# Performance work log

Hardware: AMD Instinct MI355X
Metric: run time of the kernel (lower is better)

## Reference

```python
import jax, jax.numpy as jnp
import numpy as np

DIM = 128; DSTATE = 64; DHEAD = 64; EXPAND = 2
DINNER = EXPAND * DIM; NH = DINNER // DHEAD
CONVK = 4; CHUNK = 128
BATCH = 1; DD = 32; HH = 32; WW = 32
CONVCH = DINNER + 2 * DSTATE
DPROJ = 2 * DINNER + 2 * DSTATE + NH


def rmsnorm(v, w, eps=1e-6):
    return v * jax.lax.rsqrt(jnp.mean(v * v, axis=-1, keepdims=True) + eps) * w


def ssd(xh, dt, A, Bm, Cm):
    # chunked SSD selective scan. xh [b,l,h,p], dt [b,l,h], A [h], Bm/Cm [b,l,n]
    b, l, h, p = xh.shape
    n = Bm.shape[-1]
    c, k = l // CHUNK, CHUNK
    dA = (dt * A).reshape(b, c, k, h)
    xdt = (xh * dt[..., None]).reshape(b, c, k, h, p)
    Bm = Bm.reshape(b, c, k, n)
    Cm = Cm.reshape(b, c, k, n)
    cum = jnp.cumsum(dA, axis=2)                  # [b,c,k,h] inclusive
    cum_h = cum.transpose(0, 1, 3, 2)             # [b,c,h,k]
    tri = jnp.tril(jnp.ones((k, k), bool))
    Lmat = jnp.exp(jnp.where(tri, cum_h[..., :, None] - cum_h[..., None, :], -jnp.inf))
    CB = jnp.einsum('bctn,bcsn->bcts', Cm, Bm)
    Y_intra = jnp.einsum('bcts,bchts,bcshp->bcthp', CB, Lmat, xdt)
    decay_end = jnp.exp(cum[:, :, -1:, :] - cum)  # [b,c,k,h]
    S = jnp.einsum('bcsn,bcsh,bcshp->bchpn', Bm, decay_end, xdt)
    cdec = jnp.exp(cum[:, :, -1])                 # [b,c,h]

    def step(hprev, inp):
        s_c, dec = inp
        return dec[:, :, None, None] * hprev + s_c, hprev

    init = jnp.zeros((b, h, p, n), xh.dtype)
    _, hprevs = jax.lax.scan(step, init, (S.transpose(1, 0, 2, 3, 4), cdec.transpose(1, 0, 2)))
    hprevs = hprevs.transpose(1, 0, 2, 3, 4)      # [b,c,h,p,n] state at each chunk start
    Y_inter = jnp.einsum('bctn,bcth,bchpn->bcthp', Cm, jnp.exp(cum), hprevs)
    return (Y_intra + Y_inter).reshape(b, l, h, p)


def mamba2(x, Win, convw, convb, dtb, Alog, Dp, normw, Wout):
    b, l, _ = x.shape
    zxbcdt = x @ Win
    z = zxbcdt[..., :DINNER]
    xBC = zxbcdt[..., DINNER:DINNER + CONVCH]
    dt = zxbcdt[..., DINNER + CONVCH:]
    xc = xBC.transpose(0, 2, 1)
    xc = jax.lax.conv_general_dilated(xc, convw, (1,), [(CONVK - 1, 0)],
                                      dimension_numbers=('NCH', 'OIH', 'NCH'),
                                      feature_group_count=CONVCH)
    xBC = jax.nn.silu(xc + convb[None, :, None]).transpose(0, 2, 1)
    xh = xBC[..., :DINNER].reshape(b, l, NH, DHEAD)
    Bm = xBC[..., DINNER:DINNER + DSTATE]
    Cm = xBC[..., DINNER + DSTATE:]
    dt = jax.nn.softplus(dt + dtb)
    A = -jnp.exp(Alog)
    y = ssd(xh, dt, A, Bm, Cm) + Dp[None, None, :, None] * xh
    y = y.reshape(b, l, DINNER)
    y = rmsnorm(y * jax.nn.silu(z), normw)
    return y @ Wout


def ss3d(xn, gate_w, gate_b, ps, pn, pz):
    B, D, H, W, C = xn.shape
    x_s = xn.reshape(B, -1, C)
    x_n = jnp.transpose(xn, (0, 2, 1, 3, 4)).reshape(B, -1, C)
    x_z = jnp.transpose(xn, (0, 3, 1, 2, 4)).reshape(B, -1, C)
    o_sf = mamba2(x_s, *ps).reshape(B, D, H, W, C)
    o_sb = jnp.flip(mamba2(jnp.flip(x_s, 1), *ps), 1).reshape(B, D, H, W, C)
    o_nf = mamba2(x_n, *pn).reshape(B, H, D, W, C).transpose(0, 2, 1, 3, 4)
    o_nb = jnp.flip(mamba2(jnp.flip(x_n, 1), *pn), 1).reshape(B, H, D, W, C).transpose(0, 2, 1, 3, 4)
    o_zf = mamba2(x_z, *pz).reshape(B, W, D, H, C).transpose(0, 2, 3, 1, 4)
    o_zb = jnp.flip(mamba2(jnp.flip(x_z, 1), *pz), 1).reshape(B, W, D, H, C).transpose(0, 2, 3, 1, 4)
    stack = jnp.stack([o_sf, o_sb, o_nf, o_nb, o_zf, o_zb], axis=1)  # [B,6,D,H,W,C]
    gates = jax.nn.softmax(xn @ gate_w + gate_b, axis=-1)            # [B,D,H,W,6]
    gates = jnp.transpose(gates[..., None], (0, 4, 1, 2, 3, 5))      # [B,6,D,H,W,1]
    return (stack * gates).sum(axis=1)


def block(x, norm_w, gate_w, gate_b, ps, pn, pz, loc_dw_w, loc_dw_b, loc_pw_w, loc_pw_b,
          ca_w1, ca_b1, ca_w2, ca_b2, alpha):
    xp = jnp.transpose(x, (0, 2, 3, 4, 1))
    xn = rmsnorm(xp, norm_w)
    g = jnp.transpose(ss3d(xn, gate_w, gate_b, ps, pn, pz), (0, 4, 1, 2, 3))
    xcf = jnp.transpose(xn, (0, 4, 1, 2, 3))
    lc = jax.lax.conv_general_dilated(xcf, loc_dw_w, (1, 1, 1), [(1, 1)] * 3,
                                      dimension_numbers=('NCDHW', 'OIDHW', 'NCDHW'),
                                      feature_group_count=DIM) + loc_dw_b[None, :, None, None, None]
    lc = jax.nn.silu(jnp.einsum('bcdhw,oc->bodhw', lc, loc_pw_w) + loc_pw_b[None, :, None, None, None])
    fused = alpha * g + (1.0 - alpha) * lc
    yc = jnp.mean(fused, axis=(2, 3, 4), keepdims=True)
    yc = jnp.einsum('bcdhw,oc->bodhw', yc, ca_w1) + ca_b1[None, :, None, None, None]
    yc = jnp.where(yc >= 0, yc, 0.1 * yc)  # LeakyReLU(0.1)
    yc = jnp.einsum('bcdhw,oc->bodhw', yc, ca_w2) + ca_b2[None, :, None, None, None]
    return x + fused * jax.nn.sigmoid(yc)


def setup_inputs() -> dict:
    keys = iter(jax.random.split(jax.random.key(0), 64))

    def rn(shape, s=1.0):
        return jax.random.normal(next(keys), shape, jnp.float32) * s

    inp = {"x": rn((BATCH, DIM, DD, HH, WW))}
    inp["norm_w"] = jnp.ones((DIM,)) + rn((DIM,), 0.02)
    inp["gate_w"] = rn((DIM, 6), 0.02)
    inp["gate_b"] = jnp.zeros((6,))
    for m in ("s", "n", "zm"):
        inp[m + "_Win"] = rn((DIM, DPROJ), 0.02)
        inp[m + "_convw"] = rn((CONVCH, 1, CONVK), 0.2)
        inp[m + "_convb"] = jnp.zeros((CONVCH,))
        inp[m + "_dtb"] = rn((NH,), 0.3)
        inp[m + "_Alog"] = jnp.log(jnp.arange(1, NH + 1, dtype=jnp.float32))
        inp[m + "_D"] = jnp.ones((NH,))
        inp[m + "_normw"] = jnp.ones((DINNER,))
        inp[m + "_Wout"] = rn((DINNER, DIM), 0.02)
    inp["loc_dw_w"] = rn((DIM, 1, 3, 3, 3), 0.1)
    inp["loc_dw_b"] = jnp.zeros((DIM,))
    inp["loc_pw_w"] = rn((DIM, DIM), 0.05)
    inp["loc_pw_b"] = jnp.zeros((DIM,))
    inp["ca_w1"] = rn((DIM // 16, DIM), 0.05)
    inp["ca_b1"] = jnp.zeros((DIM // 16,))
    inp["ca_w2"] = rn((DIM, DIM // 16), 0.05)
    inp["ca_b2"] = jnp.zeros((DIM,))
    inp["alpha"] = jnp.array(0.5, jnp.float32)
    return inp


def reference(x, norm_w, gate_w, gate_b,
              s_Win, s_convw, s_convb, s_dtb, s_Alog, s_D, s_normw, s_Wout,
              n_Win, n_convw, n_convb, n_dtb, n_Alog, n_D, n_normw, n_Wout,
              zm_Win, zm_convw, zm_convb, zm_dtb, zm_Alog, zm_D, zm_normw, zm_Wout,
              loc_dw_w, loc_dw_b, loc_pw_w, loc_pw_b, ca_w1, ca_b1, ca_w2, ca_b2, alpha):
    ps = (s_Win, s_convw, s_convb, s_dtb, s_Alog, s_D, s_normw, s_Wout)
    pn = (n_Win, n_convw, n_convb, n_dtb, n_Alog, n_D, n_normw, n_Wout)
    pz = (zm_Win, zm_convw, zm_convb, zm_dtb, zm_Alog, zm_D, zm_normw, zm_Wout)
    return block(x, norm_w, gate_w, gate_b, ps, pn, pz,
                 loc_dw_w, loc_dw_b, loc_pw_w, loc_pw_b, ca_w1, ca_b1, ca_w2, ca_b2, alpha)
```

## Files before the change

### kernel.cpp

```cpp
#include <hip/hip_runtime.h>


typedef unsigned short u16;
typedef unsigned int   u32;
typedef __attribute__((ext_vector_type(8))) short short8;
typedef __attribute__((ext_vector_type(8))) _Float16 half8;
typedef __attribute__((ext_vector_type(4))) float f32x4;

#define LSEQ 32768
#define CDIM 128
#define NPROJ 644
#define CCH 384
#define DIN 256
#define NHD 4
#define CKL 128
#define NCHK 256

__device__ __forceinline__ float b2f(u16 u){ u32 x=((u32)u)<<16; float f; __builtin_memcpy(&f,&x,4); return f; }
__device__ __forceinline__ u16 f2b(float f){ u32 x; __builtin_memcpy(&x,&f,4); x += 0x7fffu + ((x>>16)&1u); return (u16)(x>>16); }
__device__ __forceinline__ u16 f2h(float v){ _Float16 h=(_Float16)v; u16 b; __builtin_memcpy(&b,&h,2); return b; }
__device__ __forceinline__ float h2f(u16 b){ _Float16 h; __builtin_memcpy(&h,&b,2); return (float)h; }
__device__ __forceinline__ void up4(uint2 v, float* o){
  union { uint2 u; _Float16 h[4]; } c; c.u = v;
  o[0]=(float)c.h[0]; o[1]=(float)c.h[1]; o[2]=(float)c.h[2]; o[3]=(float)c.h[3];
}
__device__ __forceinline__ uint2 pk4(const float* o){
  union { uint2 u; _Float16 h[4]; } c;
  c.h[0]=(_Float16)o[0]; c.h[1]=(_Float16)o[1]; c.h[2]=(_Float16)o[2]; c.h[3]=(_Float16)o[3];
  return c.u;
}
__device__ __forceinline__ float sigmoidf_(float v){ return 1.f/(1.f+__expf(-v)); }
__device__ __forceinline__ float siluf_(float v){ return v*sigmoidf_(v); }
__device__ __forceinline__ float softplusf_(float v){ return (v>20.f)? v : log1pf(__expf(v)); }

__device__ __forceinline__ int seq2sp(int t, int run){
  int te = (run&1) ? (LSEQ-1-t) : t;
  int a = te>>10, b=(te>>5)&31, c=te&31;
  int d,h,w;
  switch(run>>1){
    case 0: d=a; h=b; w=c; break;
    case 1: h=a; d=b; w=c; break;
    default: w=a; d=b; h=c; break;
  }
  return (d<<10)|(h<<5)|w;
}

__global__ void k_xn(const float* __restrict__ x, const float* __restrict__ nw, float* __restrict__ XN){
  int s = blockIdx.x*256 + threadIdx.x;
  float ss = 0.f;
  #pragma unroll 8
  for (int c=0;c<CDIM;c++){ float v=x[c*LSEQ+s]; ss += v*v; }
  float sc = rsqrtf(ss*(1.f/CDIM)+1e-6f);
  #pragma unroll 8
  for (int c=0;c<CDIM;c++){ XN[c*LSEQ+s] = x[c*LSEQ+s]*sc*nw[c]; }
}

__global__ void k_gates(const float* __restrict__ XN, const float* __restrict__ gw, const float* __restrict__ gb, float* __restrict__ G){
  int s = blockIdx.x*256 + threadIdx.x;
  float a[6];
  #pragma unroll
  for (int j=0;j<6;j++) a[j]=gb[j];
  for (int c=0;c<CDIM;c++){
    float v = XN[c*LSEQ+s];
    #pragma unroll
    for (int j=0;j<6;j++) a[j] += v*gw[c*6+j];
  }
  float m=a[0];
  #pragma unroll
  for (int j=1;j<6;j++) m = fmaxf(m,a[j]);
  float e[6], ssum=0.f;
  #pragma unroll
  for (int j=0;j<6;j++){ e[j]=__expf(a[j]-m); ssum+=e[j]; }
  float inv = 1.f/ssum;
  #pragma unroll
  for (int j=0;j<6;j++) G[j*LSEQ+s] = e[j]*inv;
}

__global__ __launch_bounds__(256) void k_permute(const float* __restrict__ XN, u16* __restrict__ XNT, int dir){
  __shared__ u16 TS[128*34];
  int a = blockIdx.x>>5, b = blockIdx.x&31;
  int tid = threadIdx.x;
  int spa = (dir==1)? b : a;
  int spb = (dir==1)? a : b;
  int spbase = spa*1024 + spb*32;
  for (int idx=tid; idx<4096; idx+=256){
    int c = idx>>5, i = idx&31;
    TS[c*34+i] = f2b(XN[c*LSEQ + spbase + i]);
  }
  __syncthreads();
  for (int idx=tid; idx<4096; idx+=256){
    int i = idx>>7, c = idx&127;
    int t = (dir==2) ? (i*1024 + a*32 + b) : (a*1024 + b*32 + i);
    XNT[t*128 + c] = TS[c*34+i];
  }
}

__global__ void k_prepw(const float* __restrict__ Win, u16* __restrict__ WinT){
  int idx = blockIdx.x*256 + threadIdx.x;
  int j = idx>>7, k = idx&127;
  float v = (j<NPROJ)? Win[k*NPROJ + j] : 0.f;
  WinT[idx] = f2b(v);
}

__global__ void k_prewo(const float* __restrict__ Wout, u16* __restrict__ WoT){
  int idx = blockIdx.x*256 + threadIdx.x;
  int c = idx>>8, k = idx&255;
  WoT[idx] = f2h(Wout[k*CDIM + c]);
}

__global__ __launch_bounds__(256) void k_gin_mfma(const u16* __restrict__ XNT, const u16* __restrict__ WinT,
                                                  u16* __restrict__ ZX, int flip){
  __shared__ u16 Asb[128*136];
  __shared__ u16 Bsb[128*136];
  int j0 = blockIdx.x*128, t0 = blockIdx.y*128;
  int tid = threadIdx.x;
  for (int ch = tid; ch < 2048; ch += 256){
    int row = ch>>4, c8 = ch&15;
    int tg = flip ? (LSEQ-1-(t0+row)) : (t0+row);
    uint4 av = *(const uint4*)(XNT + tg*128 + c8*8);
    *(uint4*)(&Asb[row*136 + c8*8]) = av;
    uint4 bv = *(const uint4*)(WinT + (j0+row)*128 + c8*8);
    *(uint4*)(&Bsb[row*136 + c8*8]) = bv;
  }
  __syncthreads();
  int lane = tid&63, wid = tid>>6;
  int wm = (wid>>1)*64, wn = (wid&1)*64;
  int lm = lane&15, lq = lane>>4;
  f32x4 acc[4][4] = {};
  for (int kt=0; kt<4; kt++){
    short8 af[4], bf[4];
    #pragma unroll
    for (int mt=0;mt<4;mt++) af[mt] = *(const short8*)(&Asb[(wm+mt*16+lm)*136 + kt*32 + lq*8]);
    #pragma unroll
    for (int nt=0;nt<4;nt++) bf[nt] = *(const short8*)(&Bsb[(wn+nt*16+lm)*136 + kt*32 + lq*8]);
    #pragma unroll
    for (int mt=0;mt<4;mt++)
      #pragma unroll
      for (int nt=0;nt<4;nt++)
        acc[mt][nt] = __builtin_amdgcn_mfma_f32_16x16x32_bf16(af[mt], bf[nt], acc[mt][nt], 0,0,0);
  }
  #pragma unroll
  for (int mt=0;mt<4;mt++){
    #pragma unroll
    for (int nt=0;nt<4;nt++){
      int j = j0 + wn + nt*16 + lm;
      if (j < NPROJ){
        #pragma unroll
        for (int r=0;r<4;r++){
          int t = t0 + wm + mt*16 + lq*4 + r;
          ZX[t*NPROJ + j] = f2h(acc[mt][nt][r]);
        }
      }
    }
  }
}

__global__ __launch_bounds__(384) void k_conv(const u16* __restrict__ ZX, const float* __restrict__ cw,
                                              const float* __restrict__ cb, u16* __restrict__ XB){
  __shared__ u16 smc[35*384];
  int t0 = blockIdx.x*32;
  int tid = threadIdx.x;
  for (int idx=tid; idx<13440; idx+=384){
    int j = idx/384, chh = idx - j*384;
    int t = t0-3+j;
    smc[idx] = (t>=0)? ZX[t*NPROJ + 256 + chh] : (u16)0;
  }
  __syncthreads();
  int ch = tid;
  float w0=cw[ch*4], w1=cw[ch*4+1], w2=cw[ch*4+2], w3=cw[ch*4+3], bb=cb[ch];
  for (int i=0;i<32;i++){
    float acc = w0*h2f(smc[i*384+ch]) + w1*h2f(smc[(i+1)*384+ch])
              + w2*h2f(smc[(i+2)*384+ch]) + w3*h2f(smc[(i+3)*384+ch]) + bb;
    XB[(t0+i)*CCH + ch] = f2h(siluf_(acc));
  }
}

__global__ __launch_bounds__(256) void k_dtcum(const u16* __restrict__ ZX, const float* __restrict__ dtb,
                                               const float* __restrict__ Alog, float* __restrict__ DT,
                                               float* __restrict__ CUM, float* __restrict__ CDEC,
                                               float* __restrict__ DE){
  int g = blockIdx.x*4 + (threadIdx.x>>6);
  int lane = threadIdx.x&63;
  int c = g>>2, h = g&3;
  float A = -__expf(Alog[h]);
  float bias = dtb[h];
  int t0 = c*CKL + lane*2;
  float x0 = h2f(ZX[t0*NPROJ + 640 + h]);
  float x1 = h2f(ZX[(t0+1)*NPROJ + 640 + h]);
  float d0 = softplusf_(x0+bias), d1 = softplusf_(x1+bias);
  DT[t0*4+h] = d0; DT[(t0+1)*4+h] = d1;
  float e0 = d0*A, e1 = d1*A;
  float s = e0+e1;
  #pragma unroll
  for (int off=1; off<64; off<<=1){
    float v = __shfl_up(s, off, 64);
    if (lane>=off) s += v;
  }
  float c0 = s - e1, c1 = s;
  CUM[t0*4+h] = c0;
  CUM[(t0+1)*4+h] = c1;
  float tot = __shfl(s, 63, 64);
  DE[t0*4+h]     = __expf(tot - c0);
  DE[(t0+1)*4+h] = __expf(tot - c1);
  if (lane==0) CDEC[c*4+h] = __expf(tot);
}

__global__ __launch_bounds__(256,4) void k_chunk(const u16* __restrict__ XB, const float* __restrict__ DT,
                                                 const float* __restrict__ CUM, const float* __restrict__ DE,
                                                 const float* __restrict__ Dp,
                                                 u16* __restrict__ YA, u16* __restrict__ ST){
  __shared__ u16 sh[19968];
  u16* R0   = sh;
  u16* Cs   = sh;
  u16* Bs   = sh + 5120;
  u16* Mtri = sh;
  u16* Xsh  = sh + 11264;

  int bid = blockIdx.x; int c = bid&255, h = bid>>8;
  int tid = threadIdx.x, lane = tid&63, wid = tid>>6;
  int lm = lane&15, lq = lane>>4;
  const u16* XBc = XB + c*CKL*CCH;
  const float* DTc = DT + c*CKL*4 + h;
  const float* DEc = DE + c*CKL*4 + h;

  for (int idx=tid; idx<4096; idx+=256){
    int t2 = idx>>6, n = idx&63, t = t2*2;
    const u16* r0 = XBc + t*CCH;
    float dt0 = DTc[t*4], dt1 = DTc[(t+1)*4];
    u32 xp = (u32)f2h(h2f(r0[(h<<6)+n])*dt0) | ((u32)f2h(h2f(r0[CCH+(h<<6)+n])*dt1)<<16);
    *(u32*)&Xsh[n*136 + t] = xp;
    float de0 = DEc[t*4], de1 = DEc[(t+1)*4];
    u32 bp = (u32)f2h(h2f(r0[256+n])*de0) | ((u32)f2h(h2f(r0[CCH+256+n])*de1)<<16);
    *(u32*)&R0[n*136 + t] = bp;
  }
  if (tid<128) ((float*)(Xsh + (tid>>1)*136 + 128))[tid&1] = CUM[(c*CKL+tid)*4 + h];
  __syncthreads();
  #define CUMS(t) (((const float*)(Xsh + ((t)>>1)*136 + 128))[(t)&1])

  uint4 stg[4];
  #pragma unroll
  for (int q=0;q<4;q++){
    int idx = tid + q*256;
    int mat = idx>>9, r = (idx>>2)&127, qq = idx&3;
    stg[q] = *(const uint4*)(XBc + r*CCH + (mat? 256:320) + qq*8);
  }
  f32x4 sa[4] = {};
  #pragma unroll
  for (int kt=0; kt<4; kt++){
    half8 aa = *(const half8*)&Xsh[(wid*16+lm)*136 + kt*32 + lq*8];
    #pragma unroll
    for (int nt=0;nt<4;nt++){
      half8 bq = *(const half8*)&R0[(nt*16+lm)*136 + kt*32 + lq*8];
      sa[nt] = __builtin_amdgcn_mfma_f32_16x16x32_f16(aa, bq, sa[nt], 0,0,0);
    }
  }
  #pragma unroll
  for (int nt=0;nt<4;nt++){
    int n = nt*16 + lm;
    #pragma unroll
    for (int r=0;r<4;r++){
      int p = wid*16 + lq*4 + r;
      ST[((c*4+h)*64 + p)*64 + n] = f2h(sa[nt][r]);
    }
  }
  __syncthreads();

  #pragma unroll
  for (int q=0;q<4;q++){
    int idx = tid + q*256;
    int mat = idx>>9, r = (idx>>2)&127, qq = idx&3;
    *(uint4*)&R0[(mat?5120:0) + r*40 + qq*8] = stg[q];
  }
  __syncthreads();

  int sp0 = wid, sp1 = 7 - wid;
  #pragma unroll
  for (int q=0;q<4;q++){
    int idx = tid + q*256;
    int mat = idx>>9, r = (idx>>2)&127, qq = idx&3;
    stg[q] = *(const uint4*)(XBc + r*CCH + (mat? 256:320) + 32 + qq*8);
  }
  f32x4 cbA[4] = {};
  f32x4 cbB[8] = {};
  {
    half8 afA = *(const half8*)&Cs[(sp0*16+lm)*40 + lq*8];
    half8 afB = *(const half8*)&Cs[(sp1*16+lm)*40 + lq*8];
    #pragma unroll
    for (int st=0; st<8; st++){
      if (st <= sp1){
        half8 bq = *(const half8*)&Bs[(st*16+lm)*40 + lq*8];
        if (st <= sp0)
          cbA[st&3] = __builtin_amdgcn_mfma_f32_16x16x32_f16(afA, bq, cbA[st&3], 0,0,0);
        cbB[st] = __builtin_amdgcn_mfma_f32_16x16x32_f16(afB, bq, cbB[st], 0,0,0);
      }
    }
  }
  __syncthreads();

  #pragma unroll
  for (int q=0;q<4;q++){
    int idx = tid + q*256;
    int mat = idx>>9, r = (idx>>2)&127, qq = idx&3;
    *(uint4*)&R0[(mat?5120:0) + r*40 + qq*8] = stg[q];
  }
  __syncthreads();

  {
    half8 afA = *(const half8*)&Cs[(sp0*16+lm)*40 + lq*8];
    half8 afB = *(const half8*)&Cs[(sp1*16+lm)*40 + lq*8];
    #pragma unroll
    for (int st=0; st<8; st++){
      if (st <= sp1){
        half8 bq = *(const half8*)&Bs[(st*16+lm)*40 + lq*8];
        if (st <= sp0)
          cbA[st&3] = __builtin_amdgcn_mfma_f32_16x16x32_f16(afA, bq, cbA[st&3], 0,0,0);
        cbB[st] = __builtin_amdgcn_mfma_f32_16x16x32_f16(afB, bq, cbB[st], 0,0,0);
      }
    }
  }
  __syncthreads();

  float dval = Dp[h];
  #pragma unroll
  for (int i=0;i<2;i++){
    int sp_ = i ? sp1 : sp0;
    int q = sp_ >> 1;
    int Wst = 32*q + 40;
    int mb  = 16*(32*q*q + 48*q + (sp_&1)*(32*q+40));
    u16* Mrow = Mtri + mb;
    float ct[4];
    #pragma unroll
    for (int r=0;r<4;r++) ct[r] = CUMS(sp_*16 + lq*4 + r);

    #pragma unroll
    for (int st=0; st<8; st++){
      if (st <= sp_){
        int s = st*16 + lm;
        float cs = CUMS(s);
        f32x4 cb;
        if (i==0) cb = cbA[st&3]; else cb = cbB[st];
        if (st == sp_){
          #pragma unroll
          for (int r=0;r<4;r++){
            int t = sp_*16 + lq*4 + r;
            float m = (s <= t) ? cb[r]*__expf(ct[r]-cs) : 0.f;
            Mrow[(lq*4+r)*Wst + s] = f2h(m);
          }
          if (!(sp_&1)){
            #pragma unroll
            for (int r=0;r<4;r++) Mrow[(lq*4+r)*Wst + s + 16] = 0;
          }
        } else {
          #pragma unroll
          for (int r=0;r<4;r++)
            Mrow[(lq*4+r)*Wst + s] = f2h(cb[r]*__expf(ct[r]-cs));
        }
      }
    }

    f32x4 ya[4] = {};
    int nkt = q + 1;
    #pragma unroll
    for (int kt=0; kt<4; kt++){
      if (kt < nkt){
        half8 af = *(const half8*)&Mrow[lm*Wst + kt*32 + lq*8];
        #pragma unroll
        for (int nt=0;nt<4;nt++){
          half8 bq = *(const half8*)&Xsh[(nt*16+lm)*136 + kt*32 + lq*8];
          ya[nt] = __builtin_amdgcn_mfma_f32_16x16x32_f16(af, bq, ya[nt], 0,0,0);
        }
      }
    }

    #pragma unroll
    for (int nt=0;nt<4;nt++){
      int p = nt*16 + lm;
      #pragma unroll
      for (int r=0;r<4;r++){
        int t = sp_*16 + lq*4 + r;
        float xhv = h2f(XBc[t*CCH + (h<<6) + p]);
        YA[((c*CKL+t)<<8) + (h<<6) + p] = f2h(ya[nt][r] + dval*xhv);
      }
    }
  }
  #undef CUMS
}

__global__ void k_scan(const u16* __restrict__ ST, u16* __restrict__ HP, const float* __restrict__ CDEC){
  int g = blockIdx.x*256 + threadIdx.x;
  int h = g>>12;
  float hp = 0.f;
  #pragma unroll 8
  for (int c=0;c<NCHK;c++){
    float dec = CDEC[(c<<2)+h];
    float sv = h2f(ST[g + (c<<14)]);
    HP[g + (c<<14)] = f2h(hp);
    hp = dec*hp + sv;
  }
}

__global__ __launch_bounds__(256) void k_inter(const u16* __restrict__ XB, const float* __restrict__ CUM,
                                               const u16* __restrict__ HP, u16* __restrict__ YB){
  __shared__ u16 Cs[128*72];
  __shared__ u16 Hs[4*64*72];
  __shared__ float ex_s[4*128];
  int c = blockIdx.x;
  int tid = threadIdx.x, lane = tid&63, wid = tid>>6;
  int lm = lane&15, lq = lane>>4;
  for (int idx=tid; idx<1024; idx+=256){
    int t = idx>>3, b8 = idx&7;
    *(uint4*)&Cs[t*72 + b8*8] = *(const uint4*)(XB + (c*CKL+t)*CCH + 320 + b8*8);
  }
  for (int idx=tid; idx<2048; idx+=256){
    int h = idx>>9, p = (idx>>3)&63, b8 = idx&7;
    *(uint4*)&Hs[(h*64+p)*72 + b8*8] = *(const uint4*)(HP + ((c*4+h)*64+p)*64 + b8*8);
  }
  for (int idx=tid; idx<512; idx+=256){
    int h = idx>>7, t = idx&127;
    ex_s[h*128+t] = __expf(CUM[(c*CKL+t)*4+h]);
  }
  __syncthreads();
  int h = wid;
  const u16* Hh = &Hs[h*64*72];
  f32x4 acc[8][4] = {};
  for (int kt=0; kt<2; kt++){
    half8 af[8], bfv[4];
    #pragma unroll
    for (int mt=0;mt<8;mt++) af[mt] = *(const half8*)&Cs[(mt*16+lm)*72 + kt*32 + lq*8];
    #pragma unroll
    for (int nt=0;nt<4;nt++) bfv[nt] = *(const half8*)&Hh[(nt*16+lm)*72 + kt*32 + lq*8];
    #pragma unroll
    for (int mt=0;mt<8;mt++)
      #pragma unroll
      for (int nt=0;nt<4;nt++)
        acc[mt][nt] = __builtin_amdgcn_mfma_f32_16x16x32_f16(af[mt], bfv[nt], acc[mt][nt], 0,0,0);
  }
  #pragma unroll
  for (int mt=0;mt<8;mt++){
    #pragma unroll
    for (int r=0;r<4;r++){
      int t = mt*16 + lq*4 + r;
      float e = ex_s[h*128+t];
      u16* dst = &YB[((c*CKL+t)<<8) + (h<<6)];
      #pragma unroll
      for (int nt=0;nt<4;nt++){
        int p = nt*16 + lm;
        dst[p] = f2h(e*acc[mt][nt][r]);
      }
    }
  }
}

__global__ __launch_bounds__(256) void k_ynorm(const u16* __restrict__ YA, const u16* __restrict__ YB,
                                               const u16* __restrict__ ZX, const float* __restrict__ nw,
                                               u16* __restrict__ YH){
  int t = blockIdx.x*4 + (threadIdx.x>>6);
  int lane = threadIdx.x&63;
  float a[4], b[4], z[4], u[4];
  up4(*(const uint2*)(YA + t*DIN + lane*4), a);
  up4(*(const uint2*)(YB + t*DIN + lane*4), b);
  up4(*(const uint2*)(ZX + t*NPROJ + lane*4), z);
  float4 w = *(const float4*)(nw + lane*4);
  float ss = 0.f;
  #pragma unroll
  for (int j=0;j<4;j++){ u[j] = (a[j]+b[j])*siluf_(z[j]); ss += u[j]*u[j]; }
  #pragma unroll
  for (int off=32; off; off>>=1) ss += __shfl_xor(ss, off, 64);
  float sc = rsqrtf(ss*(1.f/DIN)+1e-6f);
  float o[4] = { u[0]*sc*w.x, u[1]*sc*w.y, u[2]*sc*w.z, u[3]*sc*w.w };
  *(uint2*)(YH + t*DIN + lane*4) = pk4(o);
}

__global__ __launch_bounds__(256) void k_gout_mfma(const u16* __restrict__ YH, const u16* __restrict__ WoT,
                                                   const float* __restrict__ G, float* __restrict__ GACC, int run){
  __shared__ u16 Ys[128*136];
  __shared__ u16 Ws[128*136];
  int t0 = blockIdx.x*128;
  int tid = threadIdx.x, lane = tid&63, wid = tid>>6;
  int lm = lane&15, lq = lane>>4;
  f32x4 acc[2][8] = {};
  for (int kb=0; kb<2; kb++){
    __syncthreads();
    for (int ch=tid; ch<2048; ch+=256){
      int row = ch>>4, c8 = ch&15;
      *(uint4*)&Ys[row*136 + c8*8] = *(const uint4*)(YH + (t0+row)*DIN + kb*128 + c8*8);
      *(uint4*)&Ws[row*136 + c8*8] = *(const uint4*)(WoT + row*DIN + kb*128 + c8*8);
    }
    __syncthreads();
    for (int kt=0; kt<4; kt++){
      half8 af[2], bfv[8];
      #pragma unroll
      for (int mt=0;mt<2;mt++) af[mt] = *(const half8*)&Ys[(wid*32+mt*16+lm)*136 + kt*32 + lq*8];
      #pragma unroll
      for (int nt=0;nt<8;nt++) bfv[nt] = *(const half8*)&Ws[(nt*16+lm)*136 + kt*32 + lq*8];
      #pragma unroll
      for (int mt=0;mt<2;mt++)
        #pragma unroll
        for (int nt=0;nt<8;nt++)
          acc[mt][nt] = __builtin_amdgcn_mfma_f32_16x16x32_f16(af[mt], bfv[nt], acc[mt][nt], 0,0,0);
    }
  }
  #pragma unroll
  for (int mt=0;mt<2;mt++){
    #pragma unroll
    for (int r=0;r<4;r++){
      int t = t0 + wid*32 + mt*16 + lq*4 + r;
      int sp = seq2sp(t, run);
      float g = G[run*LSEQ + sp];
      float* dst = &GACC[sp*CDIM];
      if (run==0){
        #pragma unroll
        for (int nt=0;nt<8;nt++) dst[nt*16+lm] = g*acc[mt][nt][r];
      } else {
        #pragma unroll
        for (int nt=0;nt<8;nt++) dst[nt*16+lm] += g*acc[mt][nt][r];
      }
    }
  }
}

__global__ __launch_bounds__(256) void k_dwconv(const float* __restrict__ XN, const float* __restrict__ w,
                                                const float* __restrict__ b, float* __restrict__ LC1){
  __shared__ float sm[3*34*40];
  int cc = blockIdx.x>>5, d = blockIdx.x&31;
  int tid = threadIdx.x;
  for (int i=tid; i<4080; i+=256) sm[i] = 0.f;
  __syncthreads();
  #pragma unroll
  for (int p=0;p<3;p++){
    int dz = d-1+p;
    if ((unsigned)dz<=31u){
      for (int idx=tid; idx<1024; idx+=256){
        int hh = idx>>5, ww = idx&31;
        sm[p*1360 + (hh+1)*40 + (ww+4)] = XN[cc*LSEQ + (dz<<10) + idx];
      }
    }
  }
  __syncthreads();
  float wreg[27];
  #pragma unroll
  for (int i=0;i<27;i++) wreg[i] = w[cc*27+i];
  float bias = b[cc];
  int h = tid>>3, w0 = (tid&7)*4;
  float4 acc = {bias,bias,bias,bias};
  #pragma unroll
  for (int p=0;p<3;p++){
    #pragma unroll
    for (int dy=0;dy<3;dy++){
      const float* row = &sm[p*1360 + (h+dy)*40 + 4];
      float left  = row[w0-1];
      float4 mid  = *(const float4*)&row[w0];
      float right = row[w0+4];
      float wa=wreg[p*9+dy*3+0], wb=wreg[p*9+dy*3+1], wc=wreg[p*9+dy*3+2];
      acc.x += wa*left  + wb*mid.x + wc*mid.y;
      acc.y += wa*mid.x + wb*mid.y + wc*mid.z;
      acc.z += wa*mid.y + wb*mid.z + wc*mid.w;
      acc.w += wa*mid.z + wb*mid.w + wc*right;
    }
  }
  *(float4*)&LC1[cc*LSEQ + (d<<10) + h*32 + w0] = acc;
}

__global__ __launch_bounds__(256) void k_pw(const float* __restrict__ LC1, const float* __restrict__ pw,
                                            const float* __restrict__ pwb, float* __restrict__ LC2){
  __shared__ u16 Ws[128*136];
  __shared__ u16 Bs[128*136];
  int s0 = blockIdx.x*128;
  int tid = threadIdx.x, lane = tid&63, wid = tid>>6;
  int lm = lane&15, lq = lane>>4;
  for (int idx=tid; idx<16384; idx+=256){
    int o = idx>>7, cc = idx&127;
    Ws[o*136+cc] = f2h(pw[idx]);
  }
  for (int idx=tid; idx<16384; idx+=256){
    int cc = idx>>7, n = idx&127;
    Bs[n*136+cc] = f2h(LC1[cc*LSEQ + s0 + n]);
  }
  __syncthreads();
  f32x4 acc[2][8] = {};
  for (int kt=0; kt<4; kt++){
    half8 af[2], bfv[8];
    #pragma unroll
    for (int mt=0;mt<2;mt++) af[mt] = *(const half8*)&Ws[(wid*32+mt*16+lm)*136 + kt*32 + lq*8];
    #pragma unroll
    for (int nt=0;nt<8;nt++) bfv[nt] = *(const half8*)&Bs[(nt*16+lm)*136 + kt*32 + lq*8];
    #pragma unroll
    for (int mt=0;mt<2;mt++)
      #pragma unroll
      for (int nt=0;nt<8;nt++)
        acc[mt][nt] = __builtin_amdgcn_mfma_f32_16x16x32_f16(af[mt], bfv[nt], acc[mt][nt], 0,0,0);
  }
  #pragma unroll
  for (int mt=0;mt<2;mt++){
    #pragma unroll
    for (int r=0;r<4;r++){
      int o = wid*32 + mt*16 + lq*4 + r;
      float bb = pwb[o];
      float* dst = &LC2[o*LSEQ + s0];
      #pragma unroll
      for (int nt=0;nt<8;nt++){
        int n = nt*16 + lm;
        dst[n] = siluf_(acc[mt][nt][r] + bb);
      }
    }
  }
}

__global__ void k_fuse(const float* __restrict__ GACC, const float* __restrict__ LC2,
                       const float* __restrict__ alpha, float* __restrict__ FUSED){
  __shared__ float tile[64*65];
  int bs = blockIdx.x>>1, bc = blockIdx.x&1;
  int s0 = bs*64, c0 = bc*64;
  int tid = threadIdx.x;
  float a = alpha[0];
  for (int idx=tid; idx<4096; idx+=256){
    int i = idx>>6, j = idx&63;
    tile[i*65+j] = GACC[(s0+i)*CDIM + c0+j];
  }
  __syncthreads();
  for (int idx=tid; idx<4096; idx+=256){
    int j = idx>>6, i = idx&63;
    float g = tile[i*65+j];
    float l = LC2[(c0+j)*LSEQ + s0+i];
    FUSED[(c0+j)*LSEQ + s0+i] = a*g + (1.f-a)*l;
  }
}

__global__ void k_mean(const float* __restrict__ F, float* __restrict__ MEAN){
  __shared__ float red[4];
  int cc = blockIdx.x, tid = threadIdx.x;
  float acc = 0.f;
  for (int s=tid; s<LSEQ; s+=256) acc += F[cc*LSEQ + s];
  #pragma unroll
  for (int off=32; off; off>>=1) acc += __shfl_down(acc, off, 64);
  if ((tid&63)==0) red[tid>>6] = acc;
  __syncthreads();
  if (tid==0) MEAN[cc] = (red[0]+red[1]+red[2]+red[3])*(1.f/LSEQ);
}

__global__ void k_ca(const float* __restrict__ MEAN, const float* __restrict__ w1, const float* __restrict__ b1,
                     const float* __restrict__ w2, const float* __restrict__ b2, float* __restrict__ SIG){
  __shared__ float y1[8];
  int tid = threadIdx.x;
  if (tid<8){
    float acc = b1[tid];
    for (int c=0;c<128;c++) acc += w1[tid*128+c]*MEAN[c];
    y1[tid] = (acc>=0.f)? acc : 0.1f*acc;
  }
  __syncthreads();
  float acc = b2[tid];
  #pragma unroll
  for (int o=0;o<8;o++) acc += w2[tid*8+o]*y1[o];
  SIG[tid] = sigmoidf_(acc);
}

__global__ void k_final(const float* __restrict__ x, const float* __restrict__ F, const float* __restrict__ SIG,
                        float* __restrict__ out){
  int idx = blockIdx.x*256 + threadIdx.x;
  int cc = idx>>15;
  out[idx] = x[idx] + F[idx]*SIG[cc];
}

extern "C" void kernel_launch(void* const* d_in, const int* in_sizes, int n_in,
                              void* d_out, int out_size, void* d_ws, size_t ws_size,
                              hipStream_t stream){
  (void)in_sizes; (void)n_in; (void)out_size; (void)ws_size;
  const float* x       = (const float*)d_in[0];
  const float* norm_w  = (const float*)d_in[1];
  const float* gate_w  = (const float*)d_in[2];
  const float* gate_b  = (const float*)d_in[3];
  const float* loc_dw_w= (const float*)d_in[28];
  const float* loc_dw_b= (const float*)d_in[29];
  const float* loc_pw_w= (const float*)d_in[30];
  const float* loc_pw_b= (const float*)d_in[31];
  const float* ca_w1   = (const float*)d_in[32];
  const float* ca_b1   = (const float*)d_in[33];
  const float* ca_w2   = (const float*)d_in[34];
  const float* ca_b2   = (const float*)d_in[35];
  const float* alpha   = (const float*)d_in[36];

  float* W     = (float*)d_ws;
  float* XN    = W;
  float* GATES = XN    + 4194304;
  float* GACC  = GATES + 196608;
  u16*   ZX    = (u16*)(GACC + 4194304);
  u16*   XB    = (u16*)(GACC + 4194304 + 10551296);
  float* DT    = GACC + 4194304 + 10551296 + 6291456;
  float* CUM   = DT    + 131072;
  float* CDEC  = CUM   + 131072;
  float* DE    = CDEC  + 1024;
  float* STreg = DE    + 131072;
  float* Y     = STreg + 4194304;
  float* LC1   = Y     + 8388608;
  float* LC2   = LC1   + 4194304;
  float* MEAN  = LC2   + 4194304;
  float* SIG   = MEAN  + 128;
  u16*   XNT   = (u16*)(SIG + 128);
  u16*   WinT  = XNT + 4194304;
  u16*   WoT   = WinT + 98304;
  u16*   ST16  = (u16*)STreg;
  u16*   YH    = (u16*)STreg;
  u16*   YA    = (u16*)Y;
  u16*   YB    = YA + 8388608;
  u16*   HP16  = (u16*)LC1;

  k_xn   <<<128,256,0,stream>>>(x, norm_w, XN);
  k_gates<<<128,256,0,stream>>>(XN, gate_w, gate_b, GATES);

  for (int r=0;r<6;r++){
    int m = r>>1;
    const float* Win   = (const float*)d_in[4 + m*8 + 0];
    const float* convw = (const float*)d_in[4 + m*8 + 1];
    const float* convb = (const float*)d_in[4 + m*8 + 2];
    const float* dtb   = (const float*)d_in[4 + m*8 + 3];
    const float* Alog  = (const float*)d_in[4 + m*8 + 4];
    const float* Dp    = (const float*)d_in[4 + m*8 + 5];
    const float* nw2   = (const float*)d_in[4 + m*8 + 6];
    const float* Wout  = (const float*)d_in[4 + m*8 + 7];
    if ((r&1)==0){
      k_permute<<<1024,256,0,stream>>>(XN, XNT, m);
      k_prepw  <<<384,256,0,stream>>>(Win, WinT);
      k_prewo  <<<128,256,0,stream>>>(Wout, WoT);
    }
    k_gin_mfma<<<dim3(6,256),256,0,stream>>>(XNT, WinT, ZX, r&1);
    k_conv    <<<1024,384,0,stream>>>(ZX, convw, convb, XB);
    k_dtcum   <<<256,256,0,stream>>>(ZX, dtb, Alog, DT, CUM, CDEC, DE);
    k_chunk   <<<1024,256,0,stream>>>(XB, DT, CUM, DE, Dp, YA, ST16);
    k_scan    <<<64,256,0,stream>>>(ST16, HP16, CDEC);
    k_inter   <<<256,256,0,stream>>>(XB, CUM, HP16, YB);
    k_ynorm   <<<8192,256,0,stream>>>(YA, YB, ZX, nw2, YH);
    k_gout_mfma<<<256,256,0,stream>>>(YH, WoT, GATES, GACC, r);
  }

  k_dwconv<<<4096,256,0,stream>>>(XN, loc_dw_w, loc_dw_b, LC1);
  k_pw    <<<256,256,0,stream>>>(LC1, loc_pw_w, loc_pw_b, LC2);
  k_fuse  <<<1024,256,0,stream>>>(GACC, LC2, alpha, LC1);
  k_mean  <<<128,256,0,stream>>>(LC1, MEAN);
  k_ca    <<<1,128,0,stream>>>(MEAN, ca_w1, ca_b1, ca_w2, ca_b2, SIG);
  k_final <<<16384,256,0,stream>>>(x, LC1, SIG, (float*)d_out);
}
```

Before: 1.084 ms.

## Fuse gate softmax, output RMSnorm, weight prep and channel mean into neighbouring kernels

Several kernels are merged. Gating is computed in the input RMSnorm pass. The two weight-transpose kernels become one launch. The gated RMSnorm of the SSM output is folded into the output-projection GEMM's tile load, with the per-row scale applied in the epilogue. The channel-mean reduction becomes atomics inside the fuse kernel, with zeroing done in dwconv. This removes launches and the YH and XN round trips, but adds redundant silu work and atomics, and makes the mean depend on float atomic ordering. The scan unroll is also raised.

```diff
diff --git a/kernel.cpp b/kernel.cpp
--- a/kernel.cpp
+++ b/kernel.cpp
@@ -45,23 +45,21 @@
   return (d<<10)|(h<<5)|w;
 }
 
-__global__ void k_xn(const float* __restrict__ x, const float* __restrict__ nw, float* __restrict__ XN){
+__global__ void k_xn(const float* __restrict__ x, const float* __restrict__ nw,
+                     const float* __restrict__ gw, const float* __restrict__ gb,
+                     float* __restrict__ XN, float* __restrict__ G){
   int s = blockIdx.x*256 + threadIdx.x;
   float ss = 0.f;
   #pragma unroll 8
   for (int c=0;c<CDIM;c++){ float v=x[c*LSEQ+s]; ss += v*v; }
   float sc = rsqrtf(ss*(1.f/CDIM)+1e-6f);
+  float a[6];
+  #pragma unroll
+  for (int j=0;j<6;j++) a[j]=gb[j];
   #pragma unroll 8
-  for (int c=0;c<CDIM;c++){ XN[c*LSEQ+s] = x[c*LSEQ+s]*sc*nw[c]; }
-}
-
-__global__ void k_gates(const float* __restrict__ XN, const float* __restrict__ gw, const float* __restrict__ gb, float* __restrict__ G){
-  int s = blockIdx.x*256 + threadIdx.x;
-  float a[6];
-  #pragma unroll
-  for (int j=0;j<6;j++) a[j]=gb[j];
   for (int c=0;c<CDIM;c++){
-    float v = XN[c*LSEQ+s];
+    float v = x[c*LSEQ+s]*sc*nw[c];
+    XN[c*LSEQ+s] = v;
     #pragma unroll
     for (int j=0;j<6;j++) a[j] += v*gw[c*6+j];
   }
@@ -95,17 +93,19 @@
   }
 }
 
-__global__ void k_prepw(const float* __restrict__ Win, u16* __restrict__ WinT){
-  int idx = blockIdx.x*256 + threadIdx.x;
-  int j = idx>>7, k = idx&127;
-  float v = (j<NPROJ)? Win[k*NPROJ + j] : 0.f;
-  WinT[idx] = f2b(v);
-}
-
-__global__ void k_prewo(const float* __restrict__ Wout, u16* __restrict__ WoT){
-  int idx = blockIdx.x*256 + threadIdx.x;
-  int c = idx>>8, k = idx&255;
-  WoT[idx] = f2h(Wout[k*CDIM + c]);
+__global__ void k_prep(const float* __restrict__ Win, const float* __restrict__ Wout,
+                       u16* __restrict__ WinT, u16* __restrict__ WoT){
+  int bid = blockIdx.x;
+  if (bid < 384){
+    int idx = bid*256 + threadIdx.x;
+    int j = idx>>7, k = idx&127;
+    float v = (j<NPROJ)? Win[k*NPROJ + j] : 0.f;
+    WinT[idx] = f2b(v);
+  } else {
+    int idx = (bid-384)*256 + threadIdx.x;
+    int c = idx>>8, k = idx&255;
+    WoT[idx] = f2h(Wout[k*CDIM + c]);
+  }
 }
 
 __global__ __launch_bounds__(256) void k_gin_mfma(const u16* __restrict__ XNT, const u16* __restrict__ WinT,
@@ -390,7 +390,7 @@
   int g = blockIdx.x*256 + threadIdx.x;
   int h = g>>12;
   float hp = 0.f;
-  #pragma unroll 8
+  #pragma unroll 32
   for (int c=0;c<NCHK;c++){
     float dec = CDEC[(c<<2)+h];
     float sv = h2f(ST[g + (c<<14)]);
@@ -451,30 +451,13 @@
   }
 }
 
-__global__ __launch_bounds__(256) void k_ynorm(const u16* __restrict__ YA, const u16* __restrict__ YB,
-                                               const u16* __restrict__ ZX, const float* __restrict__ nw,
-                                               u16* __restrict__ YH){
-  int t = blockIdx.x*4 + (threadIdx.x>>6);
-  int lane = threadIdx.x&63;
-  float a[4], b[4], z[4], u[4];
-  up4(*(const uint2*)(YA + t*DIN + lane*4), a);
-  up4(*(const uint2*)(YB + t*DIN + lane*4), b);
-  up4(*(const uint2*)(ZX + t*NPROJ + lane*4), z);
-  float4 w = *(const float4*)(nw + lane*4);
-  float ss = 0.f;
-  #pragma unroll
-  for (int j=0;j<4;j++){ u[j] = (a[j]+b[j])*siluf_(z[j]); ss += u[j]*u[j]; }
-  #pragma unroll
-  for (int off=32; off; off>>=1) ss += __shfl_xor(ss, off, 64);
-  float sc = rsqrtf(ss*(1.f/DIN)+1e-6f);
-  float o[4] = { u[0]*sc*w.x, u[1]*sc*w.y, u[2]*sc*w.z, u[3]*sc*w.w };
-  *(uint2*)(YH + t*DIN + lane*4) = pk4(o);
-}
-
-__global__ __launch_bounds__(256) void k_gout_mfma(const u16* __restrict__ YH, const u16* __restrict__ WoT,
+__global__ __launch_bounds__(256) void k_gout_mfma(const u16* __restrict__ YA, const u16* __restrict__ YB,
+                                                   const u16* __restrict__ ZX, const float* __restrict__ nw,
+                                                   const u16* __restrict__ WoT,
                                                    const float* __restrict__ G, float* __restrict__ GACC, int run){
   __shared__ u16 Ys[128*136];
   __shared__ u16 Ws[128*136];
+  __shared__ float SSs[128];
   int t0 = blockIdx.x*128;
   int tid = threadIdx.x, lane = tid&63, wid = tid>>6;
   int lm = lane&15, lq = lane>>4;
@@ -483,8 +466,31 @@
     __syncthreads();
     for (int ch=tid; ch<2048; ch+=256){
       int row = ch>>4, c8 = ch&15;
-      *(uint4*)&Ys[row*136 + c8*8] = *(const uint4*)(YH + (t0+row)*DIN + kb*128 + c8*8);
+      int t = t0+row;
+      int cb = kb*128 + c8*8;
+      uint2 av0 = *(const uint2*)(YA + t*DIN + cb);
+      uint2 av1 = *(const uint2*)(YA + t*DIN + cb + 4);
+      uint2 bv0 = *(const uint2*)(YB + t*DIN + cb);
+      uint2 bv1 = *(const uint2*)(YB + t*DIN + cb + 4);
+      uint2 zv0 = *(const uint2*)(ZX + t*NPROJ + cb);
+      uint2 zv1 = *(const uint2*)(ZX + t*NPROJ + cb + 4);
+      float af[8], bf[8], zf[8];
+      up4(av0, af); up4(av1, af+4);
+      up4(bv0, bf); up4(bv1, bf+4);
+      up4(zv0, zf); up4(zv1, zf+4);
+      float ssp = 0.f;
+      union { uint4 u; u16 h[8]; } pk;
+      #pragma unroll
+      for (int j=0;j<8;j++){
+        float u = (af[j]+bf[j])*siluf_(zf[j]);
+        ssp += u*u;
+        pk.h[j] = f2h(u*nw[cb+j]);
+      }
+      *(uint4*)&Ys[row*136 + c8*8] = pk.u;
       *(uint4*)&Ws[row*136 + c8*8] = *(const uint4*)(WoT + row*DIN + kb*128 + c8*8);
+      #pragma unroll
+      for (int off=1; off<16; off<<=1) ssp += __shfl_xor(ssp, off, 64);
+      if ((lane&15)==0){ if (kb==0) SSs[row] = ssp; else SSs[row] += ssp; }
     }
     __syncthreads();
     for (int kt=0; kt<4; kt++){
@@ -504,9 +510,11 @@
   for (int mt=0;mt<2;mt++){
     #pragma unroll
     for (int r=0;r<4;r++){
-      int t = t0 + wid*32 + mt*16 + lq*4 + r;
+      int tl = wid*32 + mt*16 + lq*4 + r;
+      int t = t0 + tl;
       int sp = seq2sp(t, run);
-      float g = G[run*LSEQ + sp];
+      float sc = rsqrtf(SSs[tl]*(1.f/DIN)+1e-6f);
+      float g = G[run*LSEQ + sp] * sc;
       float* dst = &GACC[sp*CDIM];
       if (run==0){
         #pragma unroll
@@ -520,10 +528,12 @@
 }
 
 __global__ __launch_bounds__(256) void k_dwconv(const float* __restrict__ XN, const float* __restrict__ w,
-                                                const float* __restrict__ b, float* __restrict__ LC1){
+                                                const float* __restrict__ b, float* __restrict__ LC1,
+                                                float* __restrict__ MEAN){
   __shared__ float sm[3*34*40];
   int cc = blockIdx.x>>5, d = blockIdx.x&31;
   int tid = threadIdx.x;
+  if (blockIdx.x==0 && tid<128) MEAN[tid] = 0.f;
   for (int i=tid; i<4080; i+=256) sm[i] = 0.f;
   __syncthreads();
   #pragma unroll
@@ -607,7 +617,8 @@
 }
 
 __global__ void k_fuse(const float* __restrict__ GACC, const float* __restrict__ LC2,
-                       const float* __restrict__ alpha, float* __restrict__ FUSED){
+                       const float* __restrict__ alpha, float* __restrict__ FUSED,
+                       float* __restrict__ MEAN){
   __shared__ float tile[64*65];
   int bs = blockIdx.x>>1, bc = blockIdx.x&1;
   int s0 = bs*64, c0 = bc*64;
@@ -622,20 +633,13 @@
     int j = idx>>6, i = idx&63;
     float g = tile[i*65+j];
     float l = LC2[(c0+j)*LSEQ + s0+i];
-    FUSED[(c0+j)*LSEQ + s0+i] = a*g + (1.f-a)*l;
-  }
-}
-
-__global__ void k_mean(const float* __restrict__ F, float* __restrict__ MEAN){
-  __shared__ float red[4];
-  int cc = blockIdx.x, tid = threadIdx.x;
-  float acc = 0.f;
-  for (int s=tid; s<LSEQ; s+=256) acc += F[cc*LSEQ + s];
-  #pragma unroll
-  for (int off=32; off; off>>=1) acc += __shfl_down(acc, off, 64);
-  if ((tid&63)==0) red[tid>>6] = acc;
-  __syncthreads();
-  if (tid==0) MEAN[cc] = (red[0]+red[1]+red[2]+red[3])*(1.f/LSEQ);
+    float f = a*g + (1.f-a)*l;
+    FUSED[(c0+j)*LSEQ + s0+i] = f;
+    float wsum = f;
+    #pragma unroll
+    for (int off=32; off; off>>=1) wsum += __shfl_xor(wsum, off, 64);
+    if ((tid&63)==0) atomicAdd(&MEAN[c0+j], wsum);
+  }
 }
 
 __global__ void k_ca(const float* __restrict__ MEAN, const float* __restrict__ w1, const float* __restrict__ b1,
@@ -643,8 +647,9 @@
   __shared__ float y1[8];
   int tid = threadIdx.x;
   if (tid<8){
-    float acc = b1[tid];
+    float acc = 0.f;
     for (int c=0;c<128;c++) acc += w1[tid*128+c]*MEAN[c];
+    acc = b1[tid] + acc*(1.f/LSEQ);
     y1[tid] = (acc>=0.f)? acc : 0.1f*acc;
   }
   __syncthreads();
@@ -699,13 +704,11 @@
   u16*   WinT  = XNT + 4194304;
   u16*   WoT   = WinT + 98304;
   u16*   ST16  = (u16*)STreg;
-  u16*   YH    = (u16*)STreg;
   u16*   YA    = (u16*)Y;
   u16*   YB    = YA + 8388608;
   u16*   HP16  = (u16*)LC1;
 
-  k_xn   <<<128,256,0,stream>>>(x, norm_w, XN);
-  k_gates<<<128,256,0,stream>>>(XN, gate_w, gate_b, GATES);
+  k_xn<<<128,256,0,stream>>>(x, norm_w, gate_w, gate_b, XN, GATES);
 
   for (int r=0;r<6;r++){
     int m = r>>1;
@@ -719,8 +722,7 @@
     const float* Wout  = (const float*)d_in[4 + m*8 + 7];
     if ((r&1)==0){
       k_permute<<<1024,256,0,stream>>>(XN, XNT, m);
-      k_prepw  <<<384,256,0,stream>>>(Win, WinT);
-      k_prewo  <<<128,256,0,stream>>>(Wout, WoT);
+      k_prep   <<<512,256,0,stream>>>(Win, Wout, WinT, WoT);
     }
     k_gin_mfma<<<dim3(6,256),256,0,stream>>>(XNT, WinT, ZX, r&1);
     k_conv    <<<1024,384,0,stream>>>(ZX, convw, convb, XB);
@@ -728,14 +730,12 @@
     k_chunk   <<<1024,256,0,stream>>>(XB, DT, CUM, DE, Dp, YA, ST16);
     k_scan    <<<64,256,0,stream>>>(ST16, HP16, CDEC);
     k_inter   <<<256,256,0,stream>>>(XB, CUM, HP16, YB);
-    k_ynorm   <<<8192,256,0,stream>>>(YA, YB, ZX, nw2, YH);
-    k_gout_mfma<<<256,256,0,stream>>>(YH, WoT, GATES, GACC, r);
-  }
-
-  k_dwconv<<<4096,256,0,stream>>>(XN, loc_dw_w, loc_dw_b, LC1);
+    k_gout_mfma<<<256,256,0,stream>>>(YA, YB, ZX, nw2, WoT, GATES, GACC, r);
+  }
+
+  k_dwconv<<<4096,256,0,stream>>>(XN, loc_dw_w, loc_dw_b, LC1, MEAN);
   k_pw    <<<256,256,0,stream>>>(LC1, loc_pw_w, loc_pw_b, LC2);
-  k_fuse  <<<1024,256,0,stream>>>(GACC, LC2, alpha, LC1);
-  k_mean  <<<128,256,0,stream>>>(LC1, MEAN);
+  k_fuse  <<<1024,256,0,stream>>>(GACC, LC2, alpha, LC1, MEAN);
   k_ca    <<<1,128,0,stream>>>(MEAN, ca_w1, ca_b1, ca_w2, ca_b2, SIG);
   k_final <<<16384,256,0,stream>>>(x, LC1, SIG, (float*)d_out);
 }
```

Result: slower. 1.313 ms (+21.1%).
